# Performance work log

Measured on AMD Instinct MI355X. Metric: run time of the kernel, lower is better.

The kernel has to match this reference:

```python
import jax, jax.numpy as jnp
import numpy as np

D_G, D_2D, D_3D = 512, 768, 1024
D_F, RANK, ATTN_H = 256, 16, 512
B = 8192


def _xavier(key, shape):
    fan_out, fan_in = shape
    lim = float(np.sqrt(6.0 / (fan_in + fan_out)))
    return jax.random.uniform(key, shape, jnp.float32, -lim, lim)


def setup_inputs() -> dict:
    key = jax.random.key(0)
    ks = jax.random.split(key, 12)
    inp = {
        "h_g": jax.random.normal(ks[0], (B, D_G), jnp.float32),
        "h_2d": jax.random.normal(ks[1], (B, D_2D), jnp.float32),
        "h_3d": jax.random.normal(ks[2], (B, D_3D), jnp.float32),
        # modality projections (torch Linear: y = x @ W.T + b)
        "Wg": _xavier(ks[3], (D_F, D_G)),   "bg": jnp.zeros((D_F,), jnp.float32),
        "W2": _xavier(ks[4], (D_F, D_2D)),  "b2": jnp.zeros((D_F,), jnp.float32),
        "W3": _xavier(ks[5], (D_F, D_3D)),  "b3": jnp.zeros((D_F,), jnp.float32),
        # LayerNorm affine params
        "ln_g_w": jnp.ones((D_F,), jnp.float32),  "ln_g_b": jnp.zeros((D_F,), jnp.float32),
        "ln_2_w": jnp.ones((D_F,), jnp.float32),  "ln_2_b": jnp.zeros((D_F,), jnp.float32),
        "ln_3_w": jnp.ones((D_F,), jnp.float32),  "ln_3_b": jnp.zeros((D_F,), jnp.float32),
        # rank expansions (no bias)
        "U": _xavier(ks[6], (RANK * D_F, D_F)),
        "V": _xavier(ks[7], (RANK * D_F, D_F)),
        "S": _xavier(ks[8], (RANK * D_F, D_F)),
        # attention MLP
        "Wa1": _xavier(ks[9], (ATTN_H, D_G + D_2D + D_3D)), "ba1": jnp.zeros((ATTN_H,), jnp.float32),
        "Wa2": _xavier(ks[10], (RANK, ATTN_H)),             "ba2": jnp.zeros((RANK,), jnp.float32),
    }
    return inp


def _layernorm(x, w, b, eps=1e-5):
    mu = jnp.mean(x, axis=-1, keepdims=True)
    var = jnp.var(x, axis=-1, keepdims=True)
    return (x - mu) * jax.lax.rsqrt(var + eps) * w + b


def reference(h_g, h_2d, h_3d, Wg, bg, W2, b2, W3, b3,
              ln_g_w, ln_g_b, ln_2_w, ln_2_b, ln_3_w, ln_3_b,
              U, V, S, Wa1, ba1, Wa2, ba2):
    # proj + LN + ReLU (dropout=0 / eval mode)
    g = jax.nn.relu(_layernorm(h_g @ Wg.T + bg, ln_g_w, ln_g_b))
    d2 = jax.nn.relu(_layernorm(h_2d @ W2.T + b2, ln_2_w, ln_2_b))
    d3 = jax.nn.relu(_layernorm(h_3d @ W3.T + b3, ln_3_w, ln_3_b))
    b = g.shape[0]
    # rank expansion: (B, R, d_f)
    g_r = (g @ U.T).reshape(b, RANK, D_F)
    d2_r = (d2 @ V.T).reshape(b, RANK, D_F)
    d3_r = (d3 @ S.T).reshape(b, RANK, D_F)
    z_r = g_r * d2_r * d3_r  # elementwise tri-linear product
    # rank attention from raw modality concat
    h_cat = jnp.concatenate([h_g, h_2d, h_3d], axis=-1)
    beta = jax.nn.softmax(jax.nn.relu(h_cat @ Wa1.T + ba1) @ Wa2.T + ba2, axis=-1)  # (B, R)
    z = jnp.einsum('brd,br->bd', z_r, beta)  # (B, d_f)
    return z
```

## Files before the change

kernel.cpp:

```cpp
#include <hip/hip_runtime.h>
#include <stdint.h>

#define B_ROWS 8192
#define DG 512
#define D2 768
#define D3 1024
#define DCAT 2304
#define DF 256
#define RANK 16
#define AH 512

#define OFF_WG 0
#define OFF_W2 131072
#define OFF_W3 327680
#define OFF_U  589824
#define OFF_V  1638400
#define OFF_S  2686976
#define OFF_WA1 3735552

#define WS_WBUF  0u
#define WS_HG    9830400u
#define WS_H2    18219008u
#define WS_H3    30801920u
#define WS_GBUF  9830400u
#define WS_PROJ  47579136u
#define WS_A1P   72744960u
#define WS_BETA  89522176u
#define WS_ZPART 47579136u
#define WS_REQUIRED 94240768u

typedef __attribute__((ext_vector_type(8))) short short8;
typedef __attribute__((ext_vector_type(4))) float f32x4;

__device__ inline unsigned short f2bf(float f) {
  union { float f; unsigned int u; } v; v.f = f;
  unsigned int u = v.u + 0x7fffu + ((v.u >> 16) & 1u);
  return (unsigned short)(u >> 16);
}
__device__ inline float bf2f(unsigned short h) {
  union { float f; unsigned int u; } v; v.u = ((unsigned int)h) << 16;
  return v.f;
}

typedef const unsigned int __attribute__((address_space(1)))* as1_u32p;
typedef unsigned int __attribute__((address_space(3)))* as3_u32p;

__device__ inline void g2l16(const unsigned short* g, unsigned short* l) {
  __builtin_amdgcn_global_load_lds((as1_u32p)g, (as3_u32p)l, 16, 0, 0);
}


__global__ __launch_bounds__(256) void cvt_split_k(const float* __restrict__ hg,
                                                   const float* __restrict__ h2,
                                                   const float* __restrict__ h3,
                                                   const float* __restrict__ Wg,
                                                   const float* __restrict__ W2,
                                                   const float* __restrict__ W3,
                                                   const float* __restrict__ U,
                                                   const float* __restrict__ V,
                                                   const float* __restrict__ S,
                                                   const float* __restrict__ Wa1,
                                                   unsigned short* __restrict__ hgb,
                                                   unsigned short* __restrict__ h2b,
                                                   unsigned short* __restrict__ h3b,
                                                   unsigned short* __restrict__ wbuf) {
  const int bid = blockIdx.x;
  const float* src;
  unsigned short* dst;
  int e;
  if (bid < 18432) {
    e = (bid * 256 + threadIdx.x) * 4;
    if (e < 4194304)        { src = hg + e;            dst = hgb + e; }
    else if (e < 10485760)  { src = h2 + (e - 4194304); dst = h2b + (e - 4194304); }
    else                    { src = h3 + (e - 10485760); dst = h3b + (e - 10485760); }
  } else {
    e = ((bid - 18432) * 256 + threadIdx.x) * 4;
    dst = wbuf + e;
    if (e < OFF_W2)       src = Wg  + e;
    else if (e < OFF_W3)  src = W2  + (e - OFF_W2);
    else if (e < OFF_U)   src = W3  + (e - OFF_W3);
    else if (e < OFF_V)   src = U   + (e - OFF_U);
    else if (e < OFF_S)   src = V   + (e - OFF_V);
    else if (e < OFF_WA1) src = S   + (e - OFF_S);
    else                  src = Wa1 + (e - OFF_WA1);
  }
  float4 v = *(const float4*)src;
  ushort4 o;
  o.x = f2bf(v.x); o.y = f2bf(v.y); o.z = f2bf(v.z); o.w = f2bf(v.w);
  *(ushort4*)dst = o;
}


__device__ __forceinline__ void gemm_mainloop_acc(const unsigned short* Ag, int lda,
                                                  const unsigned short* Bg, int ldb,
                                                  int K,
                                                  unsigned short* lA, unsigned short* lB,
                                                  f32x4 acc[4][4]) {
  const int tid = threadIdx.x;
  const int lane = tid & 63;
  const int wr = tid >> 7;
  const int wc = (tid >> 6) & 1;
  const int row_s = tid >> 3;
  const int kc_s = (((tid & 7) ^ ((tid >> 3) & 7)) << 3);
  const int mbase = wr * 64 + (lane & 15);
  const int nbase = wc * 64 + (lane & 15);
  const int kq = lane >> 4;
  const int h = lane & 7;

  const int nsteps = K >> 6;
  for (int ks = 0; ks < nsteps; ++ks) {
    const int k0 = ks << 6;
    __syncthreads();
#pragma unroll
    for (int p = 0; p < 4; ++p) {
      const int row = p * 32 + row_s;
      const int lofs = (p * 256 + tid) * 8;
      g2l16(Ag + (size_t)row * lda + k0 + kc_s, lA + lofs);
      g2l16(Bg + (size_t)row * ldb + k0 + kc_s, lB + lofs);
    }
    __syncthreads();
#pragma unroll
    for (int kk = 0; kk < 2; ++kk) {
      const int kch = (kk << 2) + kq;
      const int ko = ((kch ^ h) << 3);
      short8 af[4], bfr[4];
#pragma unroll
      for (int t = 0; t < 4; ++t) {
        af[t]  = *(const short8*)(lA + (mbase + t * 16) * 64 + ko);
        bfr[t] = *(const short8*)(lB + (nbase + t * 16) * 64 + ko);
      }
#pragma unroll
      for (int ti = 0; ti < 4; ++ti)
#pragma unroll
        for (int tj = 0; tj < 4; ++tj)
          acc[ti][tj] = __builtin_amdgcn_mfma_f32_16x16x32_bf16(af[ti], bfr[tj], acc[ti][tj], 0, 0, 0);
    }
  }
}

__device__ __forceinline__ void zero_acc(f32x4 acc[4][4]) {
#pragma unroll
  for (int i = 0; i < 4; ++i)
#pragma unroll
    for (int j = 0; j < 4; ++j)
      acc[i][j] = (f32x4){0.f, 0.f, 0.f, 0.f};
}


__global__ __launch_bounds__(256) void fatgemm_k(const unsigned short* __restrict__ hgb,
                                                 const unsigned short* __restrict__ h2b,
                                                 const unsigned short* __restrict__ h3b,
                                                 const unsigned short* __restrict__ wbuf,
                                                 float* __restrict__ proj,
                                                 unsigned short* __restrict__ a1part) {
  __shared__ __align__(16) unsigned short lA[128 * 64];
  __shared__ __align__(16) unsigned short lB[128 * 64];
  const int bid = blockIdx.x;
  f32x4 acc[4][4];
  const int lane = threadIdx.x & 63;
  const int wr = threadIdx.x >> 7, wc = (threadIdx.x >> 6) & 1;
  zero_acc(acc);

  if (bid < 512) {
    const int half = bid >> 8;
    const int local = bid & 255;
    const int m0 = (local >> 2) << 7;
    const int n0 = (local & 3) << 7;
    const unsigned short* Bb = wbuf + OFF_WA1 + (size_t)n0 * DCAT;
    if (half == 0) {
      gemm_mainloop_acc(hgb + (size_t)m0 * DG, DG, Bb, DCAT, DG, lA, lB, acc);
      gemm_mainloop_acc(h2b + (size_t)m0 * D2, D2, Bb + DG, DCAT, D2, lA, lB, acc);
    } else {
      gemm_mainloop_acc(h3b + (size_t)m0 * D3, D3, Bb + DG + D2, DCAT, D3, lA, lB, acc);
    }
    unsigned short* out = a1part + (size_t)half * (B_ROWS * AH);
    const int r0 = m0 + wr * 64 + ((lane >> 4) << 2);
    const int c0 = n0 + wc * 64 + (lane & 15);
#pragma unroll
    for (int ti = 0; ti < 4; ++ti)
#pragma unroll
      for (int tj = 0; tj < 4; ++tj)
#pragma unroll
        for (int i = 0; i < 4; ++i)
          out[(size_t)(r0 + ti * 16 + i) * AH + (c0 + tj * 16)] = f2bf(acc[ti][tj][i]);
  } else {
    const int b = bid - 512;
    const int z = b >> 7;
    const int local = b & 127;
    const int m0 = (local >> 1) << 7;
    const int n0 = (local & 1) << 7;
    const int Kz   = (z == 0) ? DG : (z == 1 ? D2 : D3);
    const unsigned short* Ab = (z == 0) ? hgb : (z == 1 ? h2b : h3b);
    const int woff = (z == 0) ? OFF_WG : (z == 1 ? OFF_W2 : OFF_W3);
    gemm_mainloop_acc(Ab + (size_t)m0 * Kz, Kz,
                      wbuf + woff + (size_t)n0 * Kz, Kz, Kz, lA, lB, acc);
    float* out = proj + (size_t)z * B_ROWS * DF;
    const int r0 = m0 + wr * 64 + ((lane >> 4) << 2);
    const int c0 = n0 + wc * 64 + (lane & 15);
#pragma unroll
    for (int ti = 0; ti < 4; ++ti)
#pragma unroll
      for (int tj = 0; tj < 4; ++tj)
#pragma unroll
        for (int i = 0; i < 4; ++i)
          out[(size_t)(r0 + ti * 16 + i) * DF + (c0 + tj * 16)] = acc[ti][tj][i];
  }
}


__global__ __launch_bounds__(256, 2) void rank_fused_k(const unsigned short* __restrict__ gbuf,
                                                       const unsigned short* __restrict__ wbuf,
                                                       const float* __restrict__ beta,
                                                       float* __restrict__ zpart) {
  __shared__ __align__(16) unsigned short lA[2 * 128 * 64];
  __shared__ __align__(16) unsigned short lB[2 * 128 * 64];
  __shared__ float lbeta[4 * 128];
  const int m0 = blockIdx.x * 128;
  const int d0 = blockIdx.y * 128;
  const int rg = blockIdx.z * 4;
  const int tid = threadIdx.x;

  for (int i = tid; i < 512; i += 256) {
    const int rr = i >> 7, row = i & 127;
    lbeta[i] = beta[(size_t)(m0 + row) * RANK + rg + rr];
  }
  __syncthreads();

  const int lane = tid & 63;
  const int wr = tid >> 7, wc = (tid >> 6) & 1;
  const int row_s = tid >> 3;
  const int kc_s = (((tid & 7) ^ ((tid >> 3) & 7)) << 3);
  const int mbase = wr * 64 + (lane & 15);
  const int nbase = wc * 64 + (lane & 15);
  const int kq = lane >> 4;
  const int h = lane & 7;
  const int lr0 = wr * 64 + ((lane >> 4) << 2);

  const unsigned short* Abase = gbuf + (size_t)(m0 + row_s) * DF + kc_s;
  const unsigned short* Bbase = wbuf + OFF_U + (size_t)(rg * 256 + d0 + row_s) * DF + kc_s;

  auto stage = [&](int t, unsigned short* dA, unsigned short* dB) {
    const int p = t >> 2, ks = t & 3;
    const int rr = p / 3;
    const int zi = p - rr * 3;
    const unsigned short* Ag = Abase + (size_t)zi * (B_ROWS * DF) + ks * 64;
    const unsigned short* Bg = Bbase + (size_t)zi * 1048576 + (size_t)rr * (256 * DF) + ks * 64;
#pragma unroll
    for (int q = 0; q < 4; ++q) {
      const int lofs = (q * 256 + tid) * 8;
      g2l16(Ag + (size_t)q * 32 * DF, dA + lofs);
      g2l16(Bg + (size_t)q * 32 * DF, dB + lofs);
    }
  };

  f32x4 zacc[4][4], prod[4][4], acc[4][4];
#pragma unroll
  for (int ti = 0; ti < 4; ++ti)
#pragma unroll
    for (int tj = 0; tj < 4; ++tj) {
      zacc[ti][tj] = (f32x4){0.f, 0.f, 0.f, 0.f};
      acc[ti][tj]  = (f32x4){0.f, 0.f, 0.f, 0.f};
    }

  auto compute = [&](const unsigned short* sA, const unsigned short* sB) {
#pragma unroll
    for (int kk = 0; kk < 2; ++kk) {
      const int kch = (kk << 2) + kq;
      const int ko = ((kch ^ h) << 3);
      short8 af[4], bfr[4];
#pragma unroll
      for (int t4 = 0; t4 < 4; ++t4) {
        af[t4]  = *(const short8*)(sA + (mbase + t4 * 16) * 64 + ko);
        bfr[t4] = *(const short8*)(sB + (nbase + t4 * 16) * 64 + ko);
      }
      __builtin_amdgcn_s_setprio(1);
#pragma unroll
      for (int ti = 0; ti < 4; ++ti)
#pragma unroll
        for (int tj = 0; tj < 4; ++tj)
          acc[ti][tj] = __builtin_amdgcn_mfma_f32_16x16x32_bf16(af[ti], bfr[tj], acc[ti][tj], 0, 0, 0);
      __builtin_amdgcn_s_setprio(0);
    }
  };

  stage(0, lA, lB);
  stage(1, lA + 8192, lB + 8192);

  for (int p = 0; p < 12; ++p) {
    const int rr = p / 3;
    const int zi = p - rr * 3;
#pragma unroll
    for (int ks = 0; ks < 4; ++ks) {
      const int t = (p << 2) + ks;
      const int b = t & 1;
      unsigned short* cA = lA + b * 8192;
      unsigned short* cB = lB + b * 8192;
      if (t < 47) asm volatile("s_waitcnt vmcnt(8)" ::: "memory");
      else        asm volatile("s_waitcnt vmcnt(0)" ::: "memory");
      __builtin_amdgcn_s_barrier();
      __builtin_amdgcn_sched_barrier(0);
      compute(cA, cB);
      __builtin_amdgcn_sched_barrier(0);
      __builtin_amdgcn_s_barrier();
      if (t + 2 < 48) stage(t + 2, cA, cB);
    }

    if (zi == 0) {
#pragma unroll
      for (int ti = 0; ti < 4; ++ti)
#pragma unroll
        for (int tj = 0; tj < 4; ++tj)
          prod[ti][tj] = acc[ti][tj];
    } else if (zi == 1) {
#pragma unroll
      for (int ti = 0; ti < 4; ++ti)
#pragma unroll
        for (int tj = 0; tj < 4; ++tj)
          prod[ti][tj] *= acc[ti][tj];
    } else {
#pragma unroll
      for (int ti = 0; ti < 4; ++ti) {
        const float4 b4 = *(const float4*)(lbeta + rr * 128 + lr0 + ti * 16);
        const float bv[4] = {b4.x, b4.y, b4.z, b4.w};
#pragma unroll
        for (int tj = 0; tj < 4; ++tj)
#pragma unroll
          for (int i = 0; i < 4; ++i)
            zacc[ti][tj][i] += prod[ti][tj][i] * acc[ti][tj][i] * bv[i];
      }
    }
#pragma unroll
    for (int ti = 0; ti < 4; ++ti)
#pragma unroll
      for (int tj = 0; tj < 4; ++tj)
        acc[ti][tj] = (f32x4){0.f, 0.f, 0.f, 0.f};
  }

  float* zp = zpart + (size_t)blockIdx.z * (B_ROWS * DF);
  const int c0 = d0 + wc * 64 + (lane & 15);
#pragma unroll
  for (int ti = 0; ti < 4; ++ti)
#pragma unroll
    for (int tj = 0; tj < 4; ++tj)
#pragma unroll
      for (int i = 0; i < 4; ++i)
        zp[(size_t)(m0 + lr0 + ti * 16 + i) * DF + (c0 + tj * 16)] = zacc[ti][tj][i];
}


__global__ __launch_bounds__(256) void zsum_k(const float* __restrict__ zpart,
                                              float* __restrict__ z) {
  const int idx = blockIdx.x * 256 + threadIdx.x;
  const size_t e = (size_t)idx * 4;
  const size_t stride = (size_t)B_ROWS * DF;
  float4 a = *(const float4*)(zpart + e);
  float4 b = *(const float4*)(zpart + stride + e);
  float4 c = *(const float4*)(zpart + 2 * stride + e);
  float4 d = *(const float4*)(zpart + 3 * stride + e);
  float4 o;
  o.x = (a.x + b.x) + (c.x + d.x);
  o.y = (a.y + b.y) + (c.y + d.y);
  o.z = (a.z + b.z) + (c.z + d.z);
  o.w = (a.w + b.w) + (c.w + d.w);
  *(float4*)(z + e) = o;
}


__global__ __launch_bounds__(256) void post_k(const float* __restrict__ proj,
                                              const float* __restrict__ bg, const float* __restrict__ b2, const float* __restrict__ b3,
                                              const float* __restrict__ wg, const float* __restrict__ wbg,
                                              const float* __restrict__ w2, const float* __restrict__ wb2,
                                              const float* __restrict__ w3, const float* __restrict__ wb3,
                                              unsigned short* __restrict__ gout,
                                              const unsigned short* __restrict__ a1part,
                                              const float* __restrict__ ba1,
                                              const float* __restrict__ Wa2,
                                              const float* __restrict__ ba2,
                                              float* __restrict__ beta) {
  const int bid = blockIdx.x;
  if (bid < 6144) {
    const int gid = bid * 4 + (threadIdx.x >> 6);
    const int lane = threadIdx.x & 63;
    const int z = gid >> 13;
    const int row = gid & (B_ROWS - 1);
    const float* bias = z == 0 ? bg : (z == 1 ? b2 : b3);
    const float* lw = z == 0 ? wg : (z == 1 ? w2 : w3);
    const float* lb = z == 0 ? wbg : (z == 1 ? wb2 : wb3);
    const float* x = proj + (size_t)z * B_ROWS * DF + (size_t)row * DF + lane * 4;
    float4 v = *(const float4*)x;
    float4 bb = *(const float4*)(bias + lane * 4);
    v.x += bb.x; v.y += bb.y; v.z += bb.z; v.w += bb.w;
    float s = v.x + v.y + v.z + v.w;
    float q = v.x * v.x + v.y * v.y + v.z * v.z + v.w * v.w;
#pragma unroll
    for (int m = 1; m < 64; m <<= 1) { s += __shfl_xor(s, m, 64); q += __shfl_xor(q, m, 64); }
    const float mean = s * (1.f / DF);
    const float var = q * (1.f / DF) - mean * mean;
    const float rs = rsqrtf(var + 1e-5f);
    float4 w4 = *(const float4*)(lw + lane * 4);
    float4 b4 = *(const float4*)(lb + lane * 4);
    ushort4 o;
    o.x = f2bf(fmaxf((v.x - mean) * rs * w4.x + b4.x, 0.f));
    o.y = f2bf(fmaxf((v.y - mean) * rs * w4.y + b4.y, 0.f));
    o.z = f2bf(fmaxf((v.z - mean) * rs * w4.z + b4.z, 0.f));
    o.w = f2bf(fmaxf((v.w - mean) * rs * w4.w + b4.w, 0.f));
    *(ushort4*)(gout + (size_t)z * B_ROWS * DF + (size_t)row * DF + lane * 4) = o;
  } else {
    __shared__ float lw[RANK * AH];
    for (int i = threadIdx.x; i < RANK * AH / 4; i += 256)
      *(float4*)(lw + i * 4) = *(const float4*)(Wa2 + i * 4);
    __syncthreads();
    const int lane = threadIdx.x & 63;
    const int row_base = (bid - 6144) * 16;
    float4 ca = *(const float4*)(ba1 + lane * 8);
    float4 cb = *(const float4*)(ba1 + lane * 8 + 4);
    const float bias[8] = {ca.x, ca.y, ca.z, ca.w, cb.x, cb.y, cb.z, cb.w};
#pragma unroll
    for (int it = 0; it < 4; ++it) {
      const int row = row_base + it * 4 + (threadIdx.x >> 6);
      const unsigned short* h0 = a1part + (size_t)row * AH + lane * 8;
      const unsigned short* h1 = h0 + (size_t)B_ROWS * AH;
      const uint4 p0 = *(const uint4*)h0;
      const uint4 p1 = *(const uint4*)h1;
      const unsigned int u0[4] = {p0.x, p0.y, p0.z, p0.w};
      const unsigned int u1[4] = {p1.x, p1.y, p1.z, p1.w};
      float av[8];
#pragma unroll
      for (int j = 0; j < 4; ++j) {
        const float s0 = bf2f((unsigned short)(u0[j] & 0xffffu)) + bf2f((unsigned short)(u1[j] & 0xffffu));
        const float s1 = bf2f((unsigned short)(u0[j] >> 16)) + bf2f((unsigned short)(u1[j] >> 16));
        av[2 * j]     = fmaxf(s0 + bias[2 * j], 0.f);
        av[2 * j + 1] = fmaxf(s1 + bias[2 * j + 1], 0.f);
      }
      float lg[RANK];
#pragma unroll
      for (int r = 0; r < RANK; ++r) {
        const float* wrow = lw + r * AH + lane * 8;
        float4 wa = *(const float4*)wrow;
        float4 wb = *(const float4*)(wrow + 4);
        float p = av[0] * wa.x + av[1] * wa.y + av[2] * wa.z + av[3] * wa.w
                + av[4] * wb.x + av[5] * wb.y + av[6] * wb.z + av[7] * wb.w;
#pragma unroll
        for (int m = 1; m < 64; m <<= 1) p += __shfl_xor(p, m, 64);
        lg[r] = p + ba2[r];
      }
      float mx = lg[0];
#pragma unroll
      for (int r = 1; r < RANK; ++r) mx = fmaxf(mx, lg[r]);
      float den = 0.f;
#pragma unroll
      for (int r = 0; r < RANK; ++r) { lg[r] = __expf(lg[r] - mx); den += lg[r]; }
      const float inv = 1.f / den;
      if (lane < RANK) {
        float mine = 0.f;
#pragma unroll
        for (int r = 0; r < RANK; ++r) mine = (lane == r) ? lg[r] : mine;
        beta[(size_t)row * RANK + lane] = mine * inv;
      }
    }
  }
}


extern "C" void kernel_launch(void* const* d_in, const int* in_sizes, int n_in,
                              void* d_out, int out_size, void* d_ws, size_t ws_size,
                              hipStream_t stream) {
  if (ws_size < (size_t)WS_REQUIRED) return;

  const float* h_g   = (const float*)d_in[0];
  const float* h_2d  = (const float*)d_in[1];
  const float* h_3d  = (const float*)d_in[2];
  const float* Wg    = (const float*)d_in[3];
  const float* bg    = (const float*)d_in[4];
  const float* W2    = (const float*)d_in[5];
  const float* b2    = (const float*)d_in[6];
  const float* W3    = (const float*)d_in[7];
  const float* b3    = (const float*)d_in[8];
  const float* ln_g_w = (const float*)d_in[9];
  const float* ln_g_b = (const float*)d_in[10];
  const float* ln_2_w = (const float*)d_in[11];
  const float* ln_2_b = (const float*)d_in[12];
  const float* ln_3_w = (const float*)d_in[13];
  const float* ln_3_b = (const float*)d_in[14];
  const float* U     = (const float*)d_in[15];
  const float* V     = (const float*)d_in[16];
  const float* S     = (const float*)d_in[17];
  const float* Wa1   = (const float*)d_in[18];
  const float* ba1   = (const float*)d_in[19];
  const float* Wa2   = (const float*)d_in[20];
  const float* ba2   = (const float*)d_in[21];

  char* ws = (char*)d_ws;
  unsigned short* wbuf   = (unsigned short*)(ws + WS_WBUF);
  unsigned short* hgb    = (unsigned short*)(ws + WS_HG);
  unsigned short* h2b    = (unsigned short*)(ws + WS_H2);
  unsigned short* h3b    = (unsigned short*)(ws + WS_H3);
  unsigned short* gbuf   = (unsigned short*)(ws + WS_GBUF);
  float*          proj   = (float*)(ws + WS_PROJ);
  unsigned short* a1part = (unsigned short*)(ws + WS_A1P);
  float*          beta   = (float*)(ws + WS_BETA);
  float*          zpart  = (float*)(ws + WS_ZPART);
  float* z = (float*)d_out;

  cvt_split_k<<<dim3(23232), dim3(256), 0, stream>>>(h_g, h_2d, h_3d,
                                                     Wg, W2, W3, U, V, S, Wa1,
                                                     hgb, h2b, h3b, wbuf);
  fatgemm_k<<<dim3(896), dim3(256), 0, stream>>>(hgb, h2b, h3b, wbuf, proj, a1part);
  post_k<<<dim3(6656), dim3(256), 0, stream>>>(proj, bg, b2, b3, ln_g_w, ln_g_b,
                                               ln_2_w, ln_2_b, ln_3_w, ln_3_b, gbuf,
                                               a1part, ba1, Wa2, ba2, beta);
  rank_fused_k<<<dim3(64, 2, 4), dim3(256), 0, stream>>>(gbuf, wbuf, beta, zpart);
  zsum_k<<<dim3(2048), dim3(256), 0, stream>>>(zpart, z);
}
```

Before: 313.8 us.

## Use 256x256 double-buffered GEMM tiles and fuse projection LayerNorm into epilogue

Replaces the 128x128 single-buffered GEMM with a 512-thread 256x256 tile kernel that double-buffers LDS, waits on partial vmcnt and raises wave priority around the MFMAs. The projection GEMM tiles now cover the full 256-wide feature row, so bias, LayerNorm and ReLU are applied in the epilogue through a cross-wave LDS reduction. This removes the fp32 proj buffer round trip and the separate LN pass, leaving a smaller beta-only post kernel. The trade-off is a grid of only 224 blocks for 256 CUs, which risks poor occupancy and tail imbalance, plus heavier register use from 32 accumulator tiles.

```diff
diff --git a/kernel.cpp b/kernel.cpp
--- a/kernel.cpp
+++ b/kernel.cpp
@@ -22,11 +22,10 @@
 #define WS_HG    9830400u
 #define WS_H2    18219008u
 #define WS_H3    30801920u
-#define WS_GBUF  9830400u
-#define WS_PROJ  47579136u
-#define WS_A1P   72744960u
-#define WS_BETA  89522176u
-#define WS_ZPART 47579136u
+#define WS_GBUF  47579136u
+#define WS_A1P   60162048u
+#define WS_ZPART 60162048u
+#define WS_BETA  93716480u
 #define WS_REQUIRED 94240768u
 
 typedef __attribute__((ext_vector_type(8))) short short8;
@@ -91,119 +90,183 @@
 }
 
 
-__device__ __forceinline__ void gemm_mainloop_acc(const unsigned short* Ag, int lda,
-                                                  const unsigned short* Bg, int ldb,
-                                                  int K,
-                                                  unsigned short* lA, unsigned short* lB,
-                                                  f32x4 acc[4][4]) {
+__global__ __launch_bounds__(512, 2) void fatgemm256_k(const unsigned short* __restrict__ hgb,
+                                                       const unsigned short* __restrict__ h2b,
+                                                       const unsigned short* __restrict__ h3b,
+                                                       const unsigned short* __restrict__ wbuf,
+                                                       const float* __restrict__ bg,
+                                                       const float* __restrict__ b2,
+                                                       const float* __restrict__ b3,
+                                                       const float* __restrict__ wg,
+                                                       const float* __restrict__ wbg,
+                                                       const float* __restrict__ w2,
+                                                       const float* __restrict__ wb2,
+                                                       const float* __restrict__ w3,
+                                                       const float* __restrict__ wb3,
+                                                       unsigned short* __restrict__ gout,
+                                                       unsigned short* __restrict__ a1part) {
+  __shared__ __align__(16) unsigned short lA[2 * 256 * 64];
+  __shared__ __align__(16) unsigned short lB[2 * 256 * 64];
+  const int bid = blockIdx.x;
   const int tid = threadIdx.x;
   const int lane = tid & 63;
-  const int wr = tid >> 7;
-  const int wc = (tid >> 6) & 1;
+  const int wid = tid >> 6;
+  const int wr = wid >> 2;
+  const int wc = wid & 3;
   const int row_s = tid >> 3;
-  const int kc_s = (((tid & 7) ^ ((tid >> 3) & 7)) << 3);
-  const int mbase = wr * 64 + (lane & 15);
+  const int kc_s = (((tid & 7) ^ (row_s & 7)) << 3);
+  const int mbase = wr * 128 + (lane & 15);
   const int nbase = wc * 64 + (lane & 15);
   const int kq = lane >> 4;
   const int h = lane & 7;
 
-  const int nsteps = K >> 6;
-  for (int ks = 0; ks < nsteps; ++ks) {
-    const int k0 = ks << 6;
-    __syncthreads();
-#pragma unroll
-    for (int p = 0; p < 4; ++p) {
-      const int row = p * 32 + row_s;
-      const int lofs = (p * 256 + tid) * 8;
-      g2l16(Ag + (size_t)row * lda + k0 + kc_s, lA + lofs);
-      g2l16(Bg + (size_t)row * ldb + k0 + kc_s, lB + lofs);
-    }
-    __syncthreads();
+  int role_a1 = 0, half = 0, m0 = 0, n0 = 0, z = 0, nt = 0;
+  if (bid < 64)       { role_a1 = 1; half = 0; n0 = (bid & 1) << 8; m0 = (bid >> 1) << 8; nt = 20; }
+  else if (bid < 96)  { z = 2; m0 = (bid - 64) << 8; nt = 16; }
+  else if (bid < 160) { role_a1 = 1; half = 1; int r6 = bid - 96; n0 = (r6 & 1) << 8; m0 = (r6 >> 1) << 8; nt = 16; }
+  else if (bid < 192) { z = 1; m0 = (bid - 160) << 8; nt = 12; }
+  else                { z = 0; m0 = (bid - 192) << 8; nt = 8; }
+
+  const unsigned short* projA = (z == 0) ? hgb : ((z == 1) ? h2b : h3b);
+  const int Kz   = (z == 0) ? DG : ((z == 1) ? D2 : D3);
+  const int woff = (z == 0) ? OFF_WG : ((z == 1) ? OFF_W2 : OFF_W3);
+
+  auto stage = [&](int t, unsigned short* dA, unsigned short* dB) {
+    const unsigned short* Ag; int lda; int ka;
+    const unsigned short* Bg; int ldb; int kb;
+    if (role_a1) {
+      const int tt = half ? (20 + t) : t;
+      if (tt < 8)       { Ag = hgb; lda = DG; ka = tt * 64; }
+      else if (tt < 20) { Ag = h2b; lda = D2; ka = (tt - 8) * 64; }
+      else              { Ag = h3b; lda = D3; ka = (tt - 20) * 64; }
+      Ag += (size_t)m0 * lda;
+      Bg = wbuf + OFF_WA1 + (size_t)n0 * DCAT; ldb = DCAT; kb = tt * 64;
+    } else {
+      lda = Kz; Ag = projA + (size_t)m0 * lda; ka = t * 64;
+      ldb = Kz; Bg = wbuf + woff;              kb = t * 64;
+    }
+#pragma unroll
+    for (int q = 0; q < 4; ++q) {
+      const int row = q * 64 + row_s;
+      const int lofs = (q * 512 + tid) * 8;
+      g2l16(Ag + (size_t)row * lda + ka + kc_s, dA + lofs);
+      g2l16(Bg + (size_t)row * ldb + kb + kc_s, dB + lofs);
+    }
+  };
+
+  f32x4 acc[8][4];
+#pragma unroll
+  for (int ti = 0; ti < 8; ++ti)
+#pragma unroll
+    for (int tj = 0; tj < 4; ++tj)
+      acc[ti][tj] = (f32x4){0.f, 0.f, 0.f, 0.f};
+
+  auto compute = [&](const unsigned short* sA, const unsigned short* sB) {
 #pragma unroll
     for (int kk = 0; kk < 2; ++kk) {
       const int kch = (kk << 2) + kq;
       const int ko = ((kch ^ h) << 3);
-      short8 af[4], bfr[4];
-#pragma unroll
-      for (int t = 0; t < 4; ++t) {
-        af[t]  = *(const short8*)(lA + (mbase + t * 16) * 64 + ko);
-        bfr[t] = *(const short8*)(lB + (nbase + t * 16) * 64 + ko);
-      }
-#pragma unroll
-      for (int ti = 0; ti < 4; ++ti)
+      short8 af[8], bfr[4];
+#pragma unroll
+      for (int t4 = 0; t4 < 8; ++t4)
+        af[t4] = *(const short8*)(sA + (mbase + t4 * 16) * 64 + ko);
+#pragma unroll
+      for (int t4 = 0; t4 < 4; ++t4)
+        bfr[t4] = *(const short8*)(sB + (nbase + t4 * 16) * 64 + ko);
+      __builtin_amdgcn_s_setprio(1);
+#pragma unroll
+      for (int ti = 0; ti < 8; ++ti)
 #pragma unroll
         for (int tj = 0; tj < 4; ++tj)
           acc[ti][tj] = __builtin_amdgcn_mfma_f32_16x16x32_bf16(af[ti], bfr[tj], acc[ti][tj], 0, 0, 0);
-    }
-  }
-}
-
-__device__ __forceinline__ void zero_acc(f32x4 acc[4][4]) {
-#pragma unroll
-  for (int i = 0; i < 4; ++i)
-#pragma unroll
-    for (int j = 0; j < 4; ++j)
-      acc[i][j] = (f32x4){0.f, 0.f, 0.f, 0.f};
-}
-
-
-__global__ __launch_bounds__(256) void fatgemm_k(const unsigned short* __restrict__ hgb,
-                                                 const unsigned short* __restrict__ h2b,
-                                                 const unsigned short* __restrict__ h3b,
-                                                 const unsigned short* __restrict__ wbuf,
-                                                 float* __restrict__ proj,
-                                                 unsigned short* __restrict__ a1part) {
-  __shared__ __align__(16) unsigned short lA[128 * 64];
-  __shared__ __align__(16) unsigned short lB[128 * 64];
-  const int bid = blockIdx.x;
-  f32x4 acc[4][4];
-  const int lane = threadIdx.x & 63;
-  const int wr = threadIdx.x >> 7, wc = (threadIdx.x >> 6) & 1;
-  zero_acc(acc);
-
-  if (bid < 512) {
-    const int half = bid >> 8;
-    const int local = bid & 255;
-    const int m0 = (local >> 2) << 7;
-    const int n0 = (local & 3) << 7;
-    const unsigned short* Bb = wbuf + OFF_WA1 + (size_t)n0 * DCAT;
-    if (half == 0) {
-      gemm_mainloop_acc(hgb + (size_t)m0 * DG, DG, Bb, DCAT, DG, lA, lB, acc);
-      gemm_mainloop_acc(h2b + (size_t)m0 * D2, D2, Bb + DG, DCAT, D2, lA, lB, acc);
-    } else {
-      gemm_mainloop_acc(h3b + (size_t)m0 * D3, D3, Bb + DG + D2, DCAT, D3, lA, lB, acc);
-    }
+      __builtin_amdgcn_s_setprio(0);
+    }
+  };
+
+  stage(0, lA, lB);
+  stage(1, lA + 16384, lB + 16384);
+  for (int t = 0; t < nt; ++t) {
+    const int b = t & 1;
+    unsigned short* cA = lA + b * 16384;
+    unsigned short* cB = lB + b * 16384;
+    if (t + 1 < nt) asm volatile("s_waitcnt vmcnt(8)" ::: "memory");
+    else            asm volatile("s_waitcnt vmcnt(0)" ::: "memory");
+    __builtin_amdgcn_s_barrier();
+    __builtin_amdgcn_sched_barrier(0);
+    compute(cA, cB);
+    __builtin_amdgcn_sched_barrier(0);
+    __builtin_amdgcn_s_barrier();
+    if (t + 2 < nt) stage(t + 2, cA, cB);
+  }
+
+  if (role_a1) {
     unsigned short* out = a1part + (size_t)half * (B_ROWS * AH);
-    const int r0 = m0 + wr * 64 + ((lane >> 4) << 2);
+    const int r0 = m0 + wr * 128 + ((lane >> 4) << 2);
     const int c0 = n0 + wc * 64 + (lane & 15);
 #pragma unroll
-    for (int ti = 0; ti < 4; ++ti)
+    for (int ti = 0; ti < 8; ++ti)
 #pragma unroll
       for (int tj = 0; tj < 4; ++tj)
 #pragma unroll
         for (int i = 0; i < 4; ++i)
           out[(size_t)(r0 + ti * 16 + i) * AH + (c0 + tj * 16)] = f2bf(acc[ti][tj][i]);
   } else {
-    const int b = bid - 512;
-    const int z = b >> 7;
-    const int local = b & 127;
-    const int m0 = (local >> 1) << 7;
-    const int n0 = (local & 1) << 7;
-    const int Kz   = (z == 0) ? DG : (z == 1 ? D2 : D3);
-    const unsigned short* Ab = (z == 0) ? hgb : (z == 1 ? h2b : h3b);
-    const int woff = (z == 0) ? OFF_WG : (z == 1 ? OFF_W2 : OFF_W3);
-    gemm_mainloop_acc(Ab + (size_t)m0 * Kz, Kz,
-                      wbuf + woff + (size_t)n0 * Kz, Kz, Kz, lA, lB, acc);
-    float* out = proj + (size_t)z * B_ROWS * DF;
-    const int r0 = m0 + wr * 64 + ((lane >> 4) << 2);
-    const int c0 = n0 + wc * 64 + (lane & 15);
-#pragma unroll
-    for (int ti = 0; ti < 4; ++ti)
+    const float* bias = (z == 0) ? bg : ((z == 1) ? b2 : b3);
+    const float* lnw  = (z == 0) ? wg : ((z == 1) ? w2 : w3);
+    const float* lnb  = (z == 0) ? wbg : ((z == 1) ? wb2 : wb3);
+    const int cbase = wc * 64 + (lane & 15);
+    float bs[4], lw4[4], lb4[4];
+#pragma unroll
+    for (int tj = 0; tj < 4; ++tj) {
+      const int col = cbase + tj * 16;
+      bs[tj] = bias[col]; lw4[tj] = lnw[col]; lb4[tj] = lnb[col];
+    }
+#pragma unroll
+    for (int ti = 0; ti < 8; ++ti)
 #pragma unroll
       for (int tj = 0; tj < 4; ++tj)
 #pragma unroll
         for (int i = 0; i < 4; ++i)
-          out[(size_t)(r0 + ti * 16 + i) * DF + (c0 + tj * 16)] = acc[ti][tj][i];
+          acc[ti][tj][i] += bs[tj];
+
+    float* lnr = (float*)lA;
+    __syncthreads();
+#pragma unroll
+    for (int ti = 0; ti < 8; ++ti)
+#pragma unroll
+      for (int i = 0; i < 4; ++i) {
+        float s = acc[ti][0][i] + acc[ti][1][i] + acc[ti][2][i] + acc[ti][3][i];
+        float q = acc[ti][0][i] * acc[ti][0][i] + acc[ti][1][i] * acc[ti][1][i]
+                + acc[ti][2][i] * acc[ti][2][i] + acc[ti][3][i] * acc[ti][3][i];
+#pragma unroll
+        for (int m = 1; m < 16; m <<= 1) { s += __shfl_xor(s, m, 64); q += __shfl_xor(q, m, 64); }
+        if ((lane & 15) == 0) {
+          const int rl = wr * 128 + ti * 16 + ((lane >> 4) << 2) + i;
+          lnr[rl * 8 + wc * 2]     = s;
+          lnr[rl * 8 + wc * 2 + 1] = q;
+        }
+      }
+    __syncthreads();
+    unsigned short* gz = gout + (size_t)z * (B_ROWS * DF);
+#pragma unroll
+    for (int ti = 0; ti < 8; ++ti)
+#pragma unroll
+      for (int i = 0; i < 4; ++i) {
+        const int rl = wr * 128 + ti * 16 + ((lane >> 4) << 2) + i;
+        const float4 pa = *(const float4*)(lnr + rl * 8);
+        const float4 pb = *(const float4*)(lnr + rl * 8 + 4);
+        const float sum = pa.x + pa.z + pb.x + pb.z;
+        const float sq  = pa.y + pa.w + pb.y + pb.w;
+        const float mean = sum * (1.f / DF);
+        const float var  = sq * (1.f / DF) - mean * mean;
+        const float rs   = rsqrtf(var + 1e-5f);
+        const size_t rowoff = (size_t)(m0 + rl) * DF;
+#pragma unroll
+        for (int tj = 0; tj < 4; ++tj) {
+          const float v = (acc[ti][tj][i] - mean) * rs * lw4[tj] + lb4[tj];
+          gz[rowoff + cbase + tj * 16] = f2bf(fmaxf(v, 0.f));
+        }
+      }
   }
 }
 
@@ -366,98 +429,58 @@
 }
 
 
-__global__ __launch_bounds__(256) void post_k(const float* __restrict__ proj,
-                                              const float* __restrict__ bg, const float* __restrict__ b2, const float* __restrict__ b3,
-                                              const float* __restrict__ wg, const float* __restrict__ wbg,
-                                              const float* __restrict__ w2, const float* __restrict__ wb2,
-                                              const float* __restrict__ w3, const float* __restrict__ wb3,
-                                              unsigned short* __restrict__ gout,
-                                              const unsigned short* __restrict__ a1part,
-                                              const float* __restrict__ ba1,
-                                              const float* __restrict__ Wa2,
-                                              const float* __restrict__ ba2,
-                                              float* __restrict__ beta) {
-  const int bid = blockIdx.x;
-  if (bid < 6144) {
-    const int gid = bid * 4 + (threadIdx.x >> 6);
-    const int lane = threadIdx.x & 63;
-    const int z = gid >> 13;
-    const int row = gid & (B_ROWS - 1);
-    const float* bias = z == 0 ? bg : (z == 1 ? b2 : b3);
-    const float* lw = z == 0 ? wg : (z == 1 ? w2 : w3);
-    const float* lb = z == 0 ? wbg : (z == 1 ? wb2 : wb3);
-    const float* x = proj + (size_t)z * B_ROWS * DF + (size_t)row * DF + lane * 4;
-    float4 v = *(const float4*)x;
-    float4 bb = *(const float4*)(bias + lane * 4);
-    v.x += bb.x; v.y += bb.y; v.z += bb.z; v.w += bb.w;
-    float s = v.x + v.y + v.z + v.w;
-    float q = v.x * v.x + v.y * v.y + v.z * v.z + v.w * v.w;
-#pragma unroll
-    for (int m = 1; m < 64; m <<= 1) { s += __shfl_xor(s, m, 64); q += __shfl_xor(q, m, 64); }
-    const float mean = s * (1.f / DF);
-    const float var = q * (1.f / DF) - mean * mean;
-    const float rs = rsqrtf(var + 1e-5f);
-    float4 w4 = *(const float4*)(lw + lane * 4);
-    float4 b4 = *(const float4*)(lb + lane * 4);
-    ushort4 o;
-    o.x = f2bf(fmaxf((v.x - mean) * rs * w4.x + b4.x, 0.f));
-    o.y = f2bf(fmaxf((v.y - mean) * rs * w4.y + b4.y, 0.f));
-    o.z = f2bf(fmaxf((v.z - mean) * rs * w4.z + b4.z, 0.f));
-    o.w = f2bf(fmaxf((v.w - mean) * rs * w4.w + b4.w, 0.f));
-    *(ushort4*)(gout + (size_t)z * B_ROWS * DF + (size_t)row * DF + lane * 4) = o;
-  } else {
-    __shared__ float lw[RANK * AH];
-    for (int i = threadIdx.x; i < RANK * AH / 4; i += 256)
-      *(float4*)(lw + i * 4) = *(const float4*)(Wa2 + i * 4);
-    __syncthreads();
-    const int lane = threadIdx.x & 63;
-    const int row_base = (bid - 6144) * 16;
-    float4 ca = *(const float4*)(ba1 + lane * 8);
-    float4 cb = *(const float4*)(ba1 + lane * 8 + 4);
-    const float bias[8] = {ca.x, ca.y, ca.z, ca.w, cb.x, cb.y, cb.z, cb.w};
-#pragma unroll
-    for (int it = 0; it < 4; ++it) {
-      const int row = row_base + it * 4 + (threadIdx.x >> 6);
-      const unsigned short* h0 = a1part + (size_t)row * AH + lane * 8;
-      const unsigned short* h1 = h0 + (size_t)B_ROWS * AH;
-      const uint4 p0 = *(const uint4*)h0;
-      const uint4 p1 = *(const uint4*)h1;
-      const unsigned int u0[4] = {p0.x, p0.y, p0.z, p0.w};
-      const unsigned int u1[4] = {p1.x, p1.y, p1.z, p1.w};
-      float av[8];
-#pragma unroll
-      for (int j = 0; j < 4; ++j) {
-        const float s0 = bf2f((unsigned short)(u0[j] & 0xffffu)) + bf2f((unsigned short)(u1[j] & 0xffffu));
-        const float s1 = bf2f((unsigned short)(u0[j] >> 16)) + bf2f((unsigned short)(u1[j] >> 16));
-        av[2 * j]     = fmaxf(s0 + bias[2 * j], 0.f);
-        av[2 * j + 1] = fmaxf(s1 + bias[2 * j + 1], 0.f);
-      }
-      float lg[RANK];
-#pragma unroll
-      for (int r = 0; r < RANK; ++r) {
-        const float* wrow = lw + r * AH + lane * 8;
-        float4 wa = *(const float4*)wrow;
-        float4 wb = *(const float4*)(wrow + 4);
-        float p = av[0] * wa.x + av[1] * wa.y + av[2] * wa.z + av[3] * wa.w
-                + av[4] * wb.x + av[5] * wb.y + av[6] * wb.z + av[7] * wb.w;
-#pragma unroll
-        for (int m = 1; m < 64; m <<= 1) p += __shfl_xor(p, m, 64);
-        lg[r] = p + ba2[r];
-      }
-      float mx = lg[0];
-#pragma unroll
-      for (int r = 1; r < RANK; ++r) mx = fmaxf(mx, lg[r]);
-      float den = 0.f;
-#pragma unroll
-      for (int r = 0; r < RANK; ++r) { lg[r] = __expf(lg[r] - mx); den += lg[r]; }
-      const float inv = 1.f / den;
-      if (lane < RANK) {
-        float mine = 0.f;
-#pragma unroll
-        for (int r = 0; r < RANK; ++r) mine = (lane == r) ? lg[r] : mine;
-        beta[(size_t)row * RANK + lane] = mine * inv;
-      }
-    }
+__global__ __launch_bounds__(256) void post_beta_k(const unsigned short* __restrict__ a1part,
+                                                   const float* __restrict__ ba1,
+                                                   const float* __restrict__ Wa2,
+                                                   const float* __restrict__ ba2,
+                                                   float* __restrict__ beta) {
+  __shared__ float lw[RANK * AH];
+  for (int i = threadIdx.x; i < RANK * AH / 4; i += 256)
+    *(float4*)(lw + i * 4) = *(const float4*)(Wa2 + i * 4);
+  __syncthreads();
+  const int row = blockIdx.x * 4 + (threadIdx.x >> 6);
+  const int lane = threadIdx.x & 63;
+  const unsigned short* h0 = a1part + (size_t)row * AH + lane * 8;
+  const unsigned short* h1 = h0 + (size_t)B_ROWS * AH;
+  const uint4 p0 = *(const uint4*)h0;
+  const uint4 p1 = *(const uint4*)h1;
+  const unsigned int u0[4] = {p0.x, p0.y, p0.z, p0.w};
+  const unsigned int u1[4] = {p1.x, p1.y, p1.z, p1.w};
+  float4 ca = *(const float4*)(ba1 + lane * 8);
+  float4 cb = *(const float4*)(ba1 + lane * 8 + 4);
+  const float bias[8] = {ca.x, ca.y, ca.z, ca.w, cb.x, cb.y, cb.z, cb.w};
+  float av[8];
+#pragma unroll
+  for (int j = 0; j < 4; ++j) {
+    const float s0 = bf2f((unsigned short)(u0[j] & 0xffffu)) + bf2f((unsigned short)(u1[j] & 0xffffu));
+    const float s1 = bf2f((unsigned short)(u0[j] >> 16)) + bf2f((unsigned short)(u1[j] >> 16));
+    av[2 * j]     = fmaxf(s0 + bias[2 * j], 0.f);
+    av[2 * j + 1] = fmaxf(s1 + bias[2 * j + 1], 0.f);
+  }
+  float lg[RANK];
+#pragma unroll
+  for (int r = 0; r < RANK; ++r) {
+    const float* wrow = lw + r * AH + lane * 8;
+    float4 wa = *(const float4*)wrow;
+    float4 wb = *(const float4*)(wrow + 4);
+    float p = av[0] * wa.x + av[1] * wa.y + av[2] * wa.z + av[3] * wa.w
+            + av[4] * wb.x + av[5] * wb.y + av[6] * wb.z + av[7] * wb.w;
+#pragma unroll
+    for (int m = 1; m < 64; m <<= 1) p += __shfl_xor(p, m, 64);
+    lg[r] = p + ba2[r];
+  }
+  float mx = lg[0];
+#pragma unroll
+  for (int r = 1; r < RANK; ++r) mx = fmaxf(mx, lg[r]);
+  float den = 0.f;
+#pragma unroll
+  for (int r = 0; r < RANK; ++r) { lg[r] = __expf(lg[r] - mx); den += lg[r]; }
+  const float inv = 1.f / den;
+  if (lane < RANK) {
+    float mine = 0.f;
+#pragma unroll
+    for (int r = 0; r < RANK; ++r) mine = (lane == r) ? lg[r] : mine;
+    beta[(size_t)row * RANK + lane] = mine * inv;
   }
 }
 
@@ -496,19 +519,20 @@
   unsigned short* h2b    = (unsigned short*)(ws + WS_H2);
   unsigned short* h3b    = (unsigned short*)(ws + WS_H3);
   unsigned short* gbuf   = (unsigned short*)(ws + WS_GBUF);
-  float*          proj   = (float*)(ws + WS_PROJ);
   unsigned short* a1part = (unsigned short*)(ws + WS_A1P);
+  float*          zpart  = (float*)(ws + WS_ZPART);
   float*          beta   = (float*)(ws + WS_BETA);
-  float*          zpart  = (float*)(ws + WS_ZPART);
   float* z = (float*)d_out;
 
   cvt_split_k<<<dim3(23232), dim3(256), 0, stream>>>(h_g, h_2d, h_3d,
                                                      Wg, W2, W3, U, V, S, Wa1,
                                                      hgb, h2b, h3b, wbuf);
-  fatgemm_k<<<dim3(896), dim3(256), 0, stream>>>(hgb, h2b, h3b, wbuf, proj, a1part);
-  post_k<<<dim3(6656), dim3(256), 0, stream>>>(proj, bg, b2, b3, ln_g_w, ln_g_b,
-                                               ln_2_w, ln_2_b, ln_3_w, ln_3_b, gbuf,
-                                               a1part, ba1, Wa2, ba2, beta);
+  fatgemm256_k<<<dim3(224), dim3(512), 0, stream>>>(hgb, h2b, h3b, wbuf,
+                                                    bg, b2, b3,
+                                                    ln_g_w, ln_g_b, ln_2_w, ln_2_b,
+                                                    ln_3_w, ln_3_b,
+                                                    gbuf, a1part);
+  post_beta_k<<<dim3(2048), dim3(256), 0, stream>>>(a1part, ba1, Wa2, ba2, beta);
   rank_fused_k<<<dim3(64, 2, 4), dim3(256), 0, stream>>>(gbuf, wbuf, beta, zpart);
   zsum_k<<<dim3(2048), dim3(256), 0, stream>>>(zpart, z);
 }
```

Result: faster. 296.5 us (-5.5%).
